# Performance work log

Measured on AMD Instinct MI355X. Metric: run time of the kernel, lower is better.

The kernel has to match this reference:

```python
import jax, jax.numpy as jnp
import numpy as np

D_MODEL = 4096
NUM_HEADS = 32
HEAD_DIM = D_MODEL // NUM_HEADS  # 128
Q_LAT = 12
KV_LAT = 4
B, S = 2, 2048


def setup_inputs() -> dict:
    key = jax.random.key(0)
    ks = jax.random.split(key, 6)
    sc = lambda fan_in: 1.0 / np.sqrt(fan_in)
    return {
        "x": jax.random.normal(ks[0], (B, S, D_MODEL), jnp.float32),
        "Wq_d": jax.random.normal(ks[1], (D_MODEL, Q_LAT), jnp.float32) * sc(D_MODEL),
        "bq_d": jnp.zeros((Q_LAT,), jnp.float32),
        "W_qk": jax.random.normal(ks[2], (Q_LAT, NUM_HEADS * KV_LAT), jnp.float32) * sc(Q_LAT),
        "b_qk": jnp.zeros((NUM_HEADS * KV_LAT,), jnp.float32),
        "Wkv_d": jax.random.normal(ks[3], (D_MODEL, KV_LAT), jnp.float32) * sc(D_MODEL),
        "bkv_d": jnp.zeros((KV_LAT,), jnp.float32),
        "Wv_u": jax.random.normal(ks[4], (KV_LAT, NUM_HEADS * HEAD_DIM), jnp.float32) * sc(KV_LAT),
        "bv_u": jnp.zeros((NUM_HEADS * HEAD_DIM,), jnp.float32),
        "Wo": jax.random.normal(ks[5], (NUM_HEADS * HEAD_DIM, D_MODEL), jnp.float32) * sc(NUM_HEADS * HEAD_DIM),
        "bo": jnp.zeros((D_MODEL,), jnp.float32),
    }


def reference(x, Wq_d, bq_d, W_qk, b_qk, Wkv_d, bkv_d, Wv_u, bv_u, Wo, bo):
    b, s, _ = x.shape
    # low-rank latent projections
    C_q = x @ Wq_d + bq_d                              # [B,S,Q_LAT]
    C_kv = x @ Wkv_d + bkv_d                           # [B,S,KV_LAT]
    # per-head query in kv-latent space
    q = (C_q @ W_qk + b_qk).reshape(b, s, NUM_HEADS, KV_LAT)   # [B,S,H,KV_LAT]
    # shared-key attention: keys are the compressed latent C_kv, broadcast over heads
    scores = jnp.einsum("bqhd,bkd->bhqk", q, C_kv) / jnp.sqrt(jnp.asarray(KV_LAT, x.dtype))
    attn = jax.nn.softmax(scores, axis=-1)             # [B,H,S,S]
    # up-project values from latent
    V = (C_kv @ Wv_u + bv_u).reshape(b, s, NUM_HEADS, HEAD_DIM)  # [B,S,H,Dh]
    out = jnp.einsum("bhqk,bkhd->bqhd", attn, V).reshape(b, s, NUM_HEADS * HEAD_DIM)
    return out @ Wo + bo
```

## Files before the change

kernel.cpp:

```cpp
#include <hip/hip_runtime.h>
#include <hip/hip_bf16.h>
#include <math.h>

#define D_MODEL 4096
#define NHEADS 32
#define HEAD_DIM 128
#define QLAT 12
#define KVLAT 4
#define BATCH 2
#define SEQ 2048
#define BS (BATCH*SEQ)
#define KSPLIT 2
#define KHALF (SEQ/KSPLIT)

typedef __attribute__((ext_vector_type(8))) short short8;
typedef __attribute__((ext_vector_type(4))) float f32x4;
typedef __attribute__((ext_vector_type(2))) float f32x2;

static __device__ __forceinline__ unsigned short f2bf(float f) {
    unsigned int u = __float_as_uint(f);
    unsigned int r = (u + 0x7FFFu + ((u >> 16) & 1u)) >> 16;
    return (unsigned short)r;
}

__global__ __launch_bounds__(512) void k_proj(
    const float* __restrict__ x,
    const float* __restrict__ Wq, const float* __restrict__ bq,
    const float* __restrict__ Wqk, const float* __restrict__ bqk,
    const float* __restrict__ Wkv, const float* __restrict__ bkv,
    float* __restrict__ q_s, float* __restrict__ ckv)
{
    const int t = threadIdx.x;
    const int w = t >> 6, lane = t & 63;
    const int row = blockIdx.x * 8 + w;
    const float* xr = x + (size_t)row * D_MODEL;
    float acc[16];
#pragma unroll
    for (int o = 0; o < 16; ++o) acc[o] = 0.f;

#pragma unroll 1
    for (int sweep = 0; sweep < 16; ++sweep) {
        const int i0 = sweep * 256 + lane * 4;
        float4 xv = *(const float4*)(xr + i0);
        float xa[4] = {xv.x, xv.y, xv.z, xv.w};
#pragma unroll
        for (int c = 0; c < 4; ++c) {
            const int i = i0 + c;
            const float4* wq4 = (const float4*)(Wq + (size_t)i * QLAT);
            float4 w0 = wq4[0], w1 = wq4[1], w2 = wq4[2];
            float4 wk = *(const float4*)(Wkv + (size_t)i * KVLAT);
            const float xs = xa[c];
            acc[0]  += xs * w0.x;  acc[1]  += xs * w0.y;
            acc[2]  += xs * w0.z;  acc[3]  += xs * w0.w;
            acc[4]  += xs * w1.x;  acc[5]  += xs * w1.y;
            acc[6]  += xs * w1.z;  acc[7]  += xs * w1.w;
            acc[8]  += xs * w2.x;  acc[9]  += xs * w2.y;
            acc[10] += xs * w2.z;  acc[11] += xs * w2.w;
            acc[12] += xs * wk.x;  acc[13] += xs * wk.y;
            acc[14] += xs * wk.z;  acc[15] += xs * wk.w;
        }
        __syncthreads();
    }
#pragma unroll
    for (int o = 0; o < 16; ++o) {
        float v = acc[o];
#pragma unroll
        for (int off = 32; off > 0; off >>= 1) v += __shfl_down(v, off, 64);
        acc[o] = v;
    }
    __shared__ float cq[8][QLAT];
    if (lane == 0) {
#pragma unroll
        for (int l = 0; l < QLAT; ++l) cq[w][l] = acc[l] + bq[l];
        float4 kvout;
        kvout.x = acc[12] + bkv[0]; kvout.y = acc[13] + bkv[1];
        kvout.z = acc[14] + bkv[2]; kvout.w = acc[15] + bkv[3];
        *(float4*)(ckv + (size_t)row * KVLAT) = kvout;
    }
    __syncthreads();
    if (t < 128) {
        float wq[QLAT];
#pragma unroll
        for (int l = 0; l < QLAT; ++l) wq[l] = Wqk[l * 128 + t];
        const float bb = bqk[t];
        const float SC = 0.5f * 1.44269504088896340736f;
#pragma unroll
        for (int rr = 0; rr < 8; ++rr) {
            float s = bb;
#pragma unroll
            for (int l = 0; l < QLAT; ++l) s += cq[rr][l] * wq[l];
            q_s[(size_t)(blockIdx.x * 8 + rr) * 128 + t] = s * SC;
        }
    }
}

__global__ __launch_bounds__(256) void k_attn(
    const float* __restrict__ q_s, const float* __restrict__ ckv,
    float* __restrict__ partL, float4* __restrict__ partC)
{
    const int bz = blockIdx.z;
    const int b = bz >> 1, half = bz & 1;
    const int h = blockIdx.y;
    const int s = blockIdx.x * 256 + threadIdx.x;
    __shared__ float4 kvs[KHALF];
    const float4* src = (const float4*)(ckv + ((size_t)b * SEQ + half * KHALF) * KVLAT);
    for (int k = threadIdx.x; k < KHALF; k += 256) kvs[k] = src[k];
    __syncthreads();
    const size_t r = (size_t)b * SEQ + s;
    const float4 qv = *(const float4*)(q_s + r * 128 + h * 4);
    const f32x2 q01 = {qv.x, qv.y}, q23 = {qv.z, qv.w};
    f32x2 c01 = {0.f, 0.f}, c23 = {0.f, 0.f};
    float l = 0.f;
#pragma unroll 4
    for (int k = 0; k < KHALF; ++k) {
        float4 kk = kvs[k];
        f32x2 k01 = {kk.x, kk.y}, k23 = {kk.z, kk.w};
        f32x2 d = q01 * k01 + q23 * k23;
        float sc = d.x + d.y;
        float p = exp2f(sc);
        l += p;
        c01 += k01 * p;
        c23 += k23 * p;
    }
    const size_t idx = ((size_t)(h * KSPLIT + half)) * BS + r;
    partL[idx] = l;
    float4 c; c.x = c01.x; c.y = c01.y; c.z = c23.x; c.w = c23.y;
    partC[idx] = c;
}

__global__ __launch_bounds__(256) void k_comb(
    const float* __restrict__ partL, const float4* __restrict__ partC,
    unsigned short* __restrict__ ctxb)
{
    const int tid = blockIdx.x * 256 + threadIdx.x;
    const int h = tid & (NHEADS - 1);
    const size_t r = (size_t)(tid >> 5);
    const size_t i0 = ((size_t)(h * KSPLIT)) * BS + r;
    float4 ca = partC[i0];
    float4 cb = partC[i0 + BS];
    const float l = partL[i0] + partL[i0 + BS];
    const float inv = 1.f / l;
    ushort4 o;
    o.x = f2bf((ca.x + cb.x) * inv);
    o.y = f2bf((ca.y + cb.y) * inv);
    o.z = f2bf((ca.z + cb.z) * inv);
    o.w = f2bf((ca.w + cb.w) * inv);
    *(ushort4*)(ctxb + r * 128 + h * 4) = o;
}

__global__ __launch_bounds__(256) void k_bias_init(
    const float* __restrict__ bo, float* __restrict__ biasc)
{
    int o = blockIdx.x * 256 + threadIdx.x;
    biasc[o] = bo[o];
}

__global__ __launch_bounds__(256) void k_fold(
    const float* __restrict__ Wvu, const float* __restrict__ bvu,
    const float* __restrict__ Wo, unsigned short* __restrict__ wfoldT,
    float* __restrict__ biasc)
{
    const int h = blockIdx.y;
    const int o = blockIdx.x * 256 + threadIdx.x;
    float a0 = 0.f, a1 = 0.f, a2 = 0.f, a3 = 0.f, ab = 0.f;
    const int j0 = h * HEAD_DIM;
#pragma unroll 4
    for (int d = 0; d < HEAD_DIM; ++d) {
        const int j = j0 + d;
        float wo = Wo[(size_t)j * D_MODEL + o];
        a0 += Wvu[j]             * wo;
        a1 += Wvu[D_MODEL + j]   * wo;
        a2 += Wvu[2*D_MODEL + j] * wo;
        a3 += Wvu[3*D_MODEL + j] * wo;
        ab += bvu[j] * wo;
    }
    ushort4 pk;
    pk.x = f2bf(a0); pk.y = f2bf(a1); pk.z = f2bf(a2); pk.w = f2bf(a3);
    *(ushort4*)(wfoldT + (size_t)o * 128 + h * KVLAT) = pk;
    atomicAdd(&biasc[o], ab);
}

__global__ __launch_bounds__(256) void k_out(
    const unsigned short* __restrict__ A,
    const unsigned short* __restrict__ Bt,
    const float* __restrict__ biasc, float* __restrict__ out)
{
    const int t = threadIdx.x;
    const int w = t >> 6, lane = t & 63;
    const int g = lane >> 4, lr = lane & 15;
    const int bm = blockIdx.y, bn = blockIdx.x;

    const short* Ap = (const short*)A + (size_t)(bm*64 + w*16 + lr) * 128 + g*8;
    const short* Bp = (const short*)Bt + (size_t)(bn*64 + lr) * 128 + g*8;

    f32x4 acc[4];
#pragma unroll
    for (int n = 0; n < 4; ++n) acc[n] = (f32x4){0.f, 0.f, 0.f, 0.f};

#pragma unroll
    for (int ks = 0; ks < 4; ++ks) {
        short8 a = *(const short8*)(Ap + ks*32);
#pragma unroll
        for (int n = 0; n < 4; ++n) {
            short8 b = *(const short8*)(Bp + (size_t)n*16*128 + ks*32);
            acc[n] = __builtin_amdgcn_mfma_f32_16x16x32_bf16(a, b, acc[n], 0, 0, 0);
        }
    }
    const int row0 = bm*64 + w*16 + g*4;
#pragma unroll
    for (int n = 0; n < 4; ++n) {
        const int col = bn*64 + n*16 + lr;
        const float bia = biasc[col];
#pragma unroll
        for (int reg = 0; reg < 4; ++reg)
            out[(size_t)(row0 + reg) * D_MODEL + col] = acc[n][reg] + bia;
    }
}

extern "C" void kernel_launch(void* const* d_in, const int* in_sizes, int n_in,
                              void* d_out, int out_size, void* d_ws, size_t ws_size,
                              hipStream_t stream)
{
    const float* x    = (const float*)d_in[0];
    const float* Wq   = (const float*)d_in[1];
    const float* bq   = (const float*)d_in[2];
    const float* Wqk  = (const float*)d_in[3];
    const float* bqk  = (const float*)d_in[4];
    const float* Wkv  = (const float*)d_in[5];
    const float* bkv  = (const float*)d_in[6];
    const float* Wvu  = (const float*)d_in[7];
    const float* bvu  = (const float*)d_in[8];
    const float* Wo   = (const float*)d_in[9];
    const float* bo   = (const float*)d_in[10];
    float* out = (float*)d_out;

    float* ws = (float*)d_ws;
    float* q_s   = ws;
    float* ckv   = q_s + (size_t)BS * 128;
    float* biasc = ckv + (size_t)BS * KVLAT;
    unsigned short* ctxb = (unsigned short*)(biasc + D_MODEL);
    unsigned short* wfT  = ctxb + (size_t)BS * 128;
    float4* partC = (float4*)(wfT + (size_t)D_MODEL * 128);
    float*  partL = (float*)(partC + (size_t)NHEADS * KSPLIT * BS);

    k_proj<<<BS / 8, 512, 0, stream>>>(x, Wq, bq, Wqk, bqk, Wkv, bkv, q_s, ckv);
    k_bias_init<<<D_MODEL / 256, 256, 0, stream>>>(bo, biasc);
    k_fold<<<dim3(D_MODEL / 256, NHEADS), 256, 0, stream>>>(Wvu, bvu, Wo, wfT, biasc);
    k_attn<<<dim3(SEQ / 256, NHEADS, BATCH * KSPLIT), 256, 0, stream>>>(q_s, ckv, partL, partC);
    k_comb<<<(BS * NHEADS) / 256, 256, 0, stream>>>(partL, partC, ctxb);
    k_out<<<dim3(D_MODEL / 64, BS / 64), 256, 0, stream>>>(ctxb, wfT, biasc, out);
}
```

Before: 391.7 us.

## Compute attention scores with bf16 MFMA and fuse split-K combine into attention

```diff
diff --git a/kernel.cpp b/kernel.cpp
--- a/kernel.cpp
+++ b/kernel.cpp
@@ -10,12 +10,11 @@
 #define BATCH 2
 #define SEQ 2048
 #define BS (BATCH*SEQ)
-#define KSPLIT 2
-#define KHALF (SEQ/KSPLIT)
 
 typedef __attribute__((ext_vector_type(8))) short short8;
 typedef __attribute__((ext_vector_type(4))) float f32x4;
 typedef __attribute__((ext_vector_type(2))) float f32x2;
+typedef __attribute__((ext_vector_type(4))) int int4v;
 
 static __device__ __forceinline__ unsigned short f2bf(float f) {
     unsigned int u = __float_as_uint(f);
@@ -96,56 +95,89 @@
 
 __global__ __launch_bounds__(256) void k_attn(
     const float* __restrict__ q_s, const float* __restrict__ ckv,
-    float* __restrict__ partL, float4* __restrict__ partC)
-{
-    const int bz = blockIdx.z;
-    const int b = bz >> 1, half = bz & 1;
-    const int h = blockIdx.y;
-    const int s = blockIdx.x * 256 + threadIdx.x;
-    __shared__ float4 kvs[KHALF];
-    const float4* src = (const float4*)(ckv + ((size_t)b * SEQ + half * KHALF) * KVLAT);
-    for (int k = threadIdx.x; k < KHALF; k += 256) kvs[k] = src[k];
+    unsigned short* __restrict__ ctxb)
+{
+    const int b = blockIdx.z, h = blockIdx.y;
+    const int t = threadIdx.x;
+    const int w = t >> 6, lane = t & 63;
+    const int g = lane >> 4, lr = lane & 15;
+
+    __shared__ unsigned long long Kbf[SEQ];
+    {
+        const float4* src = (const float4*)(ckv + (size_t)b * SEQ * KVLAT);
+        for (int k = t; k < SEQ; k += 256) {
+            float4 v = src[k];
+            unsigned long long lo = (unsigned long long)((unsigned)f2bf(v.x) | ((unsigned)f2bf(v.y) << 16));
+            unsigned long long hi = (unsigned long long)((unsigned)f2bf(v.z) | ((unsigned)f2bf(v.w) << 16));
+            Kbf[k] = lo | (hi << 32);
+        }
+    }
     __syncthreads();
-    const size_t r = (size_t)b * SEQ + s;
-    const float4 qv = *(const float4*)(q_s + r * 128 + h * 4);
-    const f32x2 q01 = {qv.x, qv.y}, q23 = {qv.z, qv.w};
-    f32x2 c01 = {0.f, 0.f}, c23 = {0.f, 0.f};
-    float l = 0.f;
-#pragma unroll 4
-    for (int k = 0; k < KHALF; ++k) {
-        float4 kk = kvs[k];
-        f32x2 k01 = {kk.x, kk.y}, k23 = {kk.z, kk.w};
-        f32x2 d = q01 * k01 + q23 * k23;
-        float sc = d.x + d.y;
-        float p = exp2f(sc);
-        l += p;
-        c01 += k01 * p;
-        c23 += k23 * p;
-    }
-    const size_t idx = ((size_t)(h * KSPLIT + half)) * BS + r;
-    partL[idx] = l;
-    float4 c; c.x = c01.x; c.y = c01.y; c.z = c23.x; c.w = c23.y;
-    partC[idx] = c;
-}
-
-__global__ __launch_bounds__(256) void k_comb(
-    const float* __restrict__ partL, const float4* __restrict__ partC,
-    unsigned short* __restrict__ ctxb)
-{
-    const int tid = blockIdx.x * 256 + threadIdx.x;
-    const int h = tid & (NHEADS - 1);
-    const size_t r = (size_t)(tid >> 5);
-    const size_t i0 = ((size_t)(h * KSPLIT)) * BS + r;
-    float4 ca = partC[i0];
-    float4 cb = partC[i0 + BS];
-    const float l = partL[i0] + partL[i0 + BS];
-    const float inv = 1.f / l;
-    ushort4 o;
-    o.x = f2bf((ca.x + cb.x) * inv);
-    o.y = f2bf((ca.y + cb.y) * inv);
-    o.z = f2bf((ca.z + cb.z) * inv);
-    o.w = f2bf((ca.w + cb.w) * inv);
-    *(ushort4*)(ctxb + r * 128 + h * 4) = o;
+
+    const int q0 = (blockIdx.x * 4 + w) * 16;
+    const size_t qrow = (size_t)b * SEQ + q0 + lr;
+    float4 qv = *(const float4*)(q_s + qrow * 128 + h * 4);
+    unsigned int a0 = (unsigned)f2bf(qv.x) | ((unsigned)f2bf(qv.y) << 16);
+    unsigned int a1 = (unsigned)f2bf(qv.z) | ((unsigned)f2bf(qv.w) << 16);
+    if (g != 0) { a0 = 0u; a1 = 0u; }
+    int4v ai = {(int)a0, (int)a1, 0, 0};
+    short8 afrag = __builtin_bit_cast(short8, ai);
+
+    float l0 = 0.f, l1 = 0.f, l2 = 0.f, l3 = 0.f;
+    f32x2 c0a = {0.f,0.f}, c0b = {0.f,0.f}, c1a = {0.f,0.f}, c1b = {0.f,0.f};
+    f32x2 c2a = {0.f,0.f}, c2b = {0.f,0.f}, c3a = {0.f,0.f}, c3b = {0.f,0.f};
+
+#pragma unroll 2
+    for (int it = 0; it < SEQ / 16; ++it) {
+        const int key = it * 16 + lr;
+        unsigned long long kv8 = Kbf[key];
+        unsigned int k0 = (unsigned int)kv8;
+        unsigned int k1 = (unsigned int)(kv8 >> 32);
+        unsigned int b0 = (g == 0) ? k0 : 0u;
+        unsigned int b1 = (g == 0) ? k1 : 0u;
+        int4v bi = {(int)b0, (int)b1, 0, 0};
+        short8 bfrag = __builtin_bit_cast(short8, bi);
+        f32x4 d = __builtin_amdgcn_mfma_f32_16x16x32_bf16(
+            afrag, bfrag, (f32x4){0.f,0.f,0.f,0.f}, 0, 0, 0);
+        f32x2 v01, v23;
+        v01.x = __uint_as_float(k0 << 16);
+        v01.y = __uint_as_float(k0 & 0xFFFF0000u);
+        v23.x = __uint_as_float(k1 << 16);
+        v23.y = __uint_as_float(k1 & 0xFFFF0000u);
+        float p0 = exp2f(d[0]), p1 = exp2f(d[1]), p2 = exp2f(d[2]), p3 = exp2f(d[3]);
+        l0 += p0; l1 += p1; l2 += p2; l3 += p3;
+        c0a += v01 * p0; c0b += v23 * p0;
+        c1a += v01 * p1; c1b += v23 * p1;
+        c2a += v01 * p2; c2b += v23 * p2;
+        c3a += v01 * p3; c3b += v23 * p3;
+    }
+
+#pragma unroll
+    for (int m = 1; m < 16; m <<= 1) {
+        l0 += __shfl_xor(l0, m, 64); l1 += __shfl_xor(l1, m, 64);
+        l2 += __shfl_xor(l2, m, 64); l3 += __shfl_xor(l3, m, 64);
+        c0a.x += __shfl_xor(c0a.x, m, 64); c0a.y += __shfl_xor(c0a.y, m, 64);
+        c0b.x += __shfl_xor(c0b.x, m, 64); c0b.y += __shfl_xor(c0b.y, m, 64);
+        c1a.x += __shfl_xor(c1a.x, m, 64); c1a.y += __shfl_xor(c1a.y, m, 64);
+        c1b.x += __shfl_xor(c1b.x, m, 64); c1b.y += __shfl_xor(c1b.y, m, 64);
+        c2a.x += __shfl_xor(c2a.x, m, 64); c2a.y += __shfl_xor(c2a.y, m, 64);
+        c2b.x += __shfl_xor(c2b.x, m, 64); c2b.y += __shfl_xor(c2b.y, m, 64);
+        c3a.x += __shfl_xor(c3a.x, m, 64); c3a.y += __shfl_xor(c3a.y, m, 64);
+        c3b.x += __shfl_xor(c3b.x, m, 64); c3b.y += __shfl_xor(c3b.y, m, 64);
+    }
+
+    if (lr == 0) {
+        f32x2 ca[4][2] = {{c0a,c0b},{c1a,c1b},{c2a,c2b},{c3a,c3b}};
+        float ls[4] = {l0, l1, l2, l3};
+#pragma unroll
+        for (int r = 0; r < 4; ++r) {
+            const float inv = 1.f / ls[r];
+            ushort4 o;
+            o.x = f2bf(ca[r][0].x * inv); o.y = f2bf(ca[r][0].y * inv);
+            o.z = f2bf(ca[r][1].x * inv); o.w = f2bf(ca[r][1].y * inv);
+            *(ushort4*)(ctxb + ((size_t)b * SEQ + q0 + 4 * g + r) * 128 + h * 4) = o;
+        }
+    }
 }
 
 __global__ __launch_bounds__(256) void k_bias_init(
@@ -240,13 +272,10 @@
     float* biasc = ckv + (size_t)BS * KVLAT;
     unsigned short* ctxb = (unsigned short*)(biasc + D_MODEL);
     unsigned short* wfT  = ctxb + (size_t)BS * 128;
-    float4* partC = (float4*)(wfT + (size_t)D_MODEL * 128);
-    float*  partL = (float*)(partC + (size_t)NHEADS * KSPLIT * BS);
 
     k_proj<<<BS / 8, 512, 0, stream>>>(x, Wq, bq, Wqk, bqk, Wkv, bkv, q_s, ckv);
     k_bias_init<<<D_MODEL / 256, 256, 0, stream>>>(bo, biasc);
     k_fold<<<dim3(D_MODEL / 256, NHEADS), 256, 0, stream>>>(Wvu, bvu, Wo, wfT, biasc);
-    k_attn<<<dim3(SEQ / 256, NHEADS, BATCH * KSPLIT), 256, 0, stream>>>(q_s, ckv, partL, partC);
-    k_comb<<<(BS * NHEADS) / 256, 256, 0, stream>>>(partL, partC, ctxb);
+    k_attn<<<dim3(SEQ / 64, NHEADS, BATCH), 256, 0, stream>>>(q_s, ckv, ctxb);
     k_out<<<dim3(D_MODEL / 64, BS / 64), 256, 0, stream>>>(ctxb, wfT, biasc, out);
 }
```

Result: faster. 380.7 us (-2.8%).
